# Performance work log

Measured on AMD Instinct MI355X. Metric: run time of the kernel, lower is better.

Reference implementation:

```python
import jax, jax.numpy as jnp
import numpy as np

B, N, E, H = 4, 2048, 256, 8
D = E // H
EPS = 1e-5


def _layernorm(x, g, b):
    mu = jnp.mean(x, axis=-1, keepdims=True)
    var = jnp.mean(jnp.square(x - mu), axis=-1, keepdims=True)
    return (x - mu) * jax.lax.rsqrt(var + EPS) * g + b


def setup_inputs() -> dict:
    key = jax.random.key(0)
    ks = jax.random.split(key, 8)
    s = 1.0 / np.sqrt(E)
    lin = lambda k: (jax.random.normal(k, (E, E), jnp.float32) * s)
    return {
        "x_l": jax.random.normal(ks[0], (B, N, E), jnp.float32),
        "x_r": jax.random.normal(ks[1], (B, N, E), jnp.float32),
        "Wq": lin(ks[2]), "bq": jnp.zeros((E,), jnp.float32),
        "Wk": lin(ks[3]), "bk": jnp.zeros((E,), jnp.float32),
        "Wv": lin(ks[4]), "bv": jnp.zeros((E,), jnp.float32),
        "Wp": lin(ks[5]), "bp": jnp.zeros((E,), jnp.float32),
        "ln_g": jnp.ones((E,), jnp.float32), "ln_b": jnp.zeros((E,), jnp.float32),
        "rn_g": jnp.ones((E,), jnp.float32), "rn_b": jnp.zeros((E,), jnp.float32),
    }


def reference(x_l, x_r, Wq, bq, Wk, bk, Wv, bv, Wp, bp, ln_g, ln_b, rn_g, rn_b):
    # projections -> [b, h, n, d]
    q = (x_l @ Wq + bq).reshape(B, N, H, D).transpose(0, 2, 1, 3)
    k = (x_r @ Wk + bk).reshape(B, N, H, D).transpose(0, 2, 1, 3)
    # shared value from the difference of the two streams
    v = ((x_l - x_r) @ Wv + bv).reshape(B, N, H, D).transpose(0, 2, 1, 3)

    energy = jnp.einsum('bhqd,bhkd->bhqk', q, k)  # [b,h,n,n]
    attn = jax.nn.softmax(energy / np.sqrt(D), axis=-1)  # dropout p=0 (eval)

    # attn used as-is and transposed against the SAME value tensor
    out_l = jnp.einsum('bhqk,bhkd->bhqd', attn, v)
    out_r = jnp.einsum('bhqk,bhqd->bhkd', attn, v)  # == attn^T @ v

    out_l = out_l.transpose(0, 2, 1, 3).reshape(B, N, E)
    out_r = out_r.transpose(0, 2, 1, 3).reshape(B, N, E)

    out_l = _layernorm(out_l @ Wp + bp, ln_g, ln_b) + x_l
    out_r = _layernorm(out_r @ Wp + bp, rn_g, rn_b) + x_r
    return (out_l, out_r)
```

## Files before the change

kernel.cpp:

```cpp
#include <hip/hip_runtime.h>
#include <math.h>


typedef __attribute__((ext_vector_type(8))) short short8;
typedef __attribute__((ext_vector_type(4))) float f32x4;
typedef __attribute__((ext_vector_type(16))) float f32x16;
typedef __attribute__((ext_vector_type(4))) unsigned short u16x4;

union FragU { unsigned int u[4]; short8 s8; };

__device__ __forceinline__ unsigned short bf16_rn(float f) {
    union { float f; unsigned int u; } c; c.f = f;
    return (unsigned short)((c.u + 0x7FFFu + ((c.u >> 16) & 1u)) >> 16);
}
__device__ __forceinline__ float b2f(unsigned short u) {
    union { unsigned int i; float f; } c; c.i = ((unsigned int)u) << 16;
    return c.f;
}

#if __has_builtin(__builtin_amdgcn_exp2f)
__device__ __forceinline__ float fexp2(float x) { return __builtin_amdgcn_exp2f(x); }
#else
__device__ __forceinline__ float fexp2(float x) { return exp2f(x); }
#endif

__device__ __forceinline__ f32x4 mfma16(short8 a, short8 b, f32x4 c) {
    return __builtin_amdgcn_mfma_f32_16x16x32_bf16(a, b, c, 0, 0, 0);
}
__device__ __forceinline__ f32x16 mfma32(short8 a, short8 b, f32x16 c) {
    return __builtin_amdgcn_mfma_f32_32x32x16_bf16(a, b, c, 0, 0, 0);
}

__device__ __forceinline__ void plswap(unsigned int& x, unsigned int& y) {
    asm("v_permlane32_swap_b32 %0, %1" : "+v"(x), "+v"(y));
}

__device__ __forceinline__ short8 pfrag(unsigned int w0, unsigned int w1,
                                        unsigned int w2, unsigned int w3) {
    plswap(w0, w2);
    plswap(w1, w3);
    FragU fu;
    fu.u[0] = w0; fu.u[1] = w1; fu.u[2] = w2; fu.u[3] = w3;
    return fu.s8;
}

__global__ void prep_all(const float* __restrict__ xl, const float* __restrict__ xr,
                         const float* __restrict__ Wq, const float* __restrict__ Wk,
                         const float* __restrict__ Wv, const float* __restrict__ Wp,
                         unsigned short* __restrict__ xlb, unsigned short* __restrict__ xrb,
                         unsigned short* __restrict__ xdb,
                         unsigned short* __restrict__ Wqt, unsigned short* __restrict__ Wkt,
                         unsigned short* __restrict__ Wvt, unsigned short* __restrict__ Wpt) {
    const int bid = blockIdx.x;
    if (bid < 2048) {
        const size_t i = ((size_t)bid * 256 + threadIdx.x) * 4;
        const float4 A = *(const float4*)(xl + i);
        const float4 Bv = *(const float4*)(xr + i);
        u16x4 pa = { bf16_rn(A.x), bf16_rn(A.y), bf16_rn(A.z), bf16_rn(A.w) };
        u16x4 pb = { bf16_rn(Bv.x), bf16_rn(Bv.y), bf16_rn(Bv.z), bf16_rn(Bv.w) };
        u16x4 pd = { bf16_rn(A.x - Bv.x), bf16_rn(A.y - Bv.y),
                     bf16_rn(A.z - Bv.z), bf16_rn(A.w - Bv.w) };
        *(u16x4*)(xlb + i) = pa;
        *(u16x4*)(xrb + i) = pb;
        *(u16x4*)(xdb + i) = pd;
    } else {
        const int gid = (bid - 2048) * 256 + threadIdx.x;
        const int m = gid >> 16;
        const int idx = gid & 65535;
        const int k = idx >> 8, n = idx & 255;
        const float* W = (m == 0) ? Wq : (m == 1) ? Wk : (m == 2) ? Wv : Wp;
        unsigned short* Wt = (m == 0) ? Wqt : (m == 1) ? Wkt : (m == 2) ? Wvt : Wpt;
        Wt[n * 256 + k] = bf16_rn(W[(size_t)k * 256 + n]);
    }
}

__launch_bounds__(256)
__global__ void qkv_gemm(const unsigned short* __restrict__ xlb,
                         const unsigned short* __restrict__ xrb,
                         const unsigned short* __restrict__ xdb,
                         const unsigned short* __restrict__ Wqt,
                         const unsigned short* __restrict__ Wkt,
                         const unsigned short* __restrict__ Wvt,
                         const float* __restrict__ bq, const float* __restrict__ bk,
                         const float* __restrict__ bv,
                         unsigned short* __restrict__ Qg, unsigned short* __restrict__ Kg,
                         unsigned short* __restrict__ Vtg) {
    const int z = blockIdx.z;
    const unsigned short* A  = (z == 0) ? xlb : (z == 1) ? xrb : xdb;
    const unsigned short* Wt = (z == 0) ? Wqt : (z == 1) ? Wkt : Wvt;
    const float* bias        = (z == 0) ? bq  : (z == 1) ? bk  : bv;

    __shared__ unsigned short At[2][128][40];
    __shared__ unsigned short Bt[2][64][40];

    const int tid = threadIdx.x;
    const int lane = tid & 63, wv = tid >> 6;
    const int a = lane & 15, g = lane >> 4;
    const int wr = wv >> 1, wc = wv & 1;
    const int r0 = blockIdx.x * 128;
    const int c0 = blockIdx.y * 64;

    const f32x4 fz = {0.f, 0.f, 0.f, 0.f};
    f32x4 acc[4][2];
#pragma unroll
    for (int f = 0; f < 4; ++f)
#pragma unroll
        for (int t = 0; t < 2; ++t) acc[f][t] = fz;

    const int arow = tid >> 1, aoff = (tid & 1) * 16;
    const int brow = tid >> 2, boff = (tid & 3) * 8;
    const unsigned short* asrc = A + (size_t)(r0 + arow) * 256 + aoff;
    const unsigned short* bsrc = Wt + (size_t)(c0 + brow) * 256 + boff;

#define QKV_STAGE(KS, BUF)                                                      \
    {                                                                           \
        *(short8*)&At[BUF][arow][aoff]     = *(const short8*)(asrc + (KS) * 32); \
        *(short8*)&At[BUF][arow][aoff + 8] = *(const short8*)(asrc + (KS) * 32 + 8); \
        *(short8*)&Bt[BUF][brow][boff]     = *(const short8*)(bsrc + (KS) * 32); \
    }

    QKV_STAGE(0, 0)
    __syncthreads();

#pragma unroll
    for (int ks = 0; ks < 8; ++ks) {
        const int b = ks & 1;
        if (ks < 7) QKV_STAGE(ks + 1, b ^ 1)
        short8 af[4], bfr[2];
#pragma unroll
        for (int f = 0; f < 4; ++f) af[f] = *(const short8*)&At[b][wr * 64 + f * 16 + a][g * 8];
#pragma unroll
        for (int t = 0; t < 2; ++t) bfr[t] = *(const short8*)&Bt[b][wc * 32 + t * 16 + a][g * 8];
#pragma unroll
        for (int f = 0; f < 4; ++f)
#pragma unroll
            for (int t = 0; t < 2; ++t) acc[f][t] = mfma16(af[f], bfr[t], acc[f][t]);
        __syncthreads();
    }
#undef QKV_STAGE

    const float scq = 0.17677669529663687f * 1.4426950408889634f;
#pragma unroll
    for (int t = 0; t < 2; ++t) {
        const int C = c0 + wc * 32 + t * 16 + a;
        const float bb = bias[C];
        const int h = C >> 5, d = C & 31;
#pragma unroll
        for (int f = 0; f < 4; ++f) {
            const int Rb = r0 + wr * 64 + f * 16 + g * 4;
            const int b_ = Rb >> 11, n = Rb & 2047;
            const int bhh = b_ * 8 + h;
            float v[4];
#pragma unroll
            for (int r = 0; r < 4; ++r) {
                v[r] = acc[f][t][r] + bb;
                if (z == 0) v[r] *= scq;
            }
            if (z < 2) {
                unsigned short* dst = ((z == 0) ? Qg : Kg) + (size_t)(bhh * 2048 + n) * 32 + d;
#pragma unroll
                for (int r = 0; r < 4; ++r) dst[(size_t)r * 32] = bf16_rn(v[r]);
            } else {
                u16x4 pk = { bf16_rn(v[0]), bf16_rn(v[1]), bf16_rn(v[2]), bf16_rn(v[3]) };
                *(u16x4*)(Vtg + (size_t)(bhh * 32 + d) * 2048 + n) = pk;
            }
        }
    }
}

#define P1_TILE(SB)                                                             \
    {                                                                           \
        const short8 ck0 = *(const short8*)((SB) + ro);                         \
        const short8 ck1 = *(const short8*)((SB) + 512 + ro);                   \
        const short8 cv0 = *(const short8*)((SB) + 1024 + ro);                  \
        const short8 cv1 = *(const short8*)((SB) + 1536 + ro);                  \
        f32x16 s = {};                                                          \
        s = mfma32(ck0, qf0, s);                                                \
        s = mfma32(ck1, qf1, s);                                                \
        float p[16];                                                            \
        _Pragma("unroll") for (int j = 0; j < 16; ++j) p[j] = fexp2(s[j]);      \
        l_run += (((p[0] + p[1]) + (p[2] + p[3])) + ((p[4] + p[5]) + (p[6] + p[7]))) \
               + (((p[8] + p[9]) + (p[10] + p[11])) + ((p[12] + p[13]) + (p[14] + p[15]))); \
        unsigned int w[8];                                                      \
        _Pragma("unroll") for (int mm = 0; mm < 8; ++mm)                        \
            asm("v_cvt_pk_bf16_f32 %0, %1, %2"                                  \
                : "=v"(w[mm]) : "v"(p[2 * mm]), "v"(p[2 * mm + 1]));            \
        acc = mfma32(cv0, pfrag(w[0], w[1], w[2], w[3]), acc);                  \
        acc = mfma32(cv1, pfrag(w[4], w[5], w[6], w[7]), acc);                  \
    }

__launch_bounds__(512, 4)
__global__ void attn_pass1(const unsigned short* __restrict__ Qg,
                           const unsigned short* __restrict__ Kg,
                           const unsigned short* __restrict__ Vtg,
                           unsigned short* __restrict__ AOl,
                           unsigned short* __restrict__ Vsg) {
    __shared__ unsigned short ST[2][2][2][2][2][64][8];
    __shared__ float accS[4][16][64];
    __shared__ float lsumS[4][64];

    const int f = blockIdx.x;
    const int bh = 4 * (f & 7) + (f >> 7);
    const int qblk = (f >> 3) & 15;
    const int tid = threadIdx.x;
    const int wv = tid >> 6;
    const int qi = wv & 3, z = wv >> 2;
    const int lane = tid & 63, l31 = lane & 31, hi = lane >> 5;
    const int q0 = qblk * 128 + qi * 32;

    const unsigned short* Qb = Qg + (size_t)bh * 2048 * 32;
    const unsigned short* Kb = Kg + (size_t)bh * 2048 * 32;
    const unsigned short* Vb = Vtg + (size_t)bh * 32 * 2048;

    const short8 qf0 = *(const short8*)(Qb + (size_t)(q0 + l31) * 32 + hi * 8);
    const short8 qf1 = *(const short8*)(Qb + (size_t)(q0 + l31) * 32 + 16 + hi * 8);

    const int kv = qi >> 1;
    const int srow = (qi & 1) * 16 + (lane >> 2);
    const int m = lane & 3;
    unsigned short* wp00 = &ST[z][0][0][kv][m >> 1][srow + 32 * (m & 1)][0];
    unsigned short* wp01 = &ST[z][0][1][kv][m >> 1][srow + 32 * (m & 1)][0];
    unsigned short* wp10 = &ST[z][1][0][kv][m >> 1][srow + 32 * (m & 1)][0];
    unsigned short* wp11 = &ST[z][1][1][kv][m >> 1][srow + 32 * (m & 1)][0];
    const size_t gstep = kv ? 32 : 1024;
    const unsigned short* sgb = kv
        ? Vb + (size_t)srow * 2048 + m * 8
        : Kb + (size_t)srow * 32 + m * 8;
    const int zt = z * 32;

    const unsigned short* rb00 = &ST[z][0][0][0][0][0][0];
    const unsigned short* rb01 = &ST[z][0][1][0][0][0][0];
    const unsigned short* rb10 = &ST[z][1][0][0][0][0][0];
    const unsigned short* rb11 = &ST[z][1][1][0][0][0][0];
    const int ro = (l31 + 32 * hi) * 8;

    f32x16 acc = {};
    float l_run = 0.f;

    short8 rr0 = *(const short8*)(sgb + (size_t)(zt + 0) * gstep);
    short8 rr1 = *(const short8*)(sgb + (size_t)(zt + 1) * gstep);
    *(short8*)wp00 = rr0;
    *(short8*)wp01 = rr1;
    rr0 = *(const short8*)(sgb + (size_t)(zt + 2) * gstep);
    rr1 = *(const short8*)(sgb + (size_t)(zt + 3) * gstep);
    __syncthreads();

#pragma unroll
    for (int ph = 0; ph < 16; ++ph) {
        const int pb = ph & 1;
        unsigned short* wA = pb ? wp00 : wp10;
        unsigned short* wB = pb ? wp01 : wp11;
        const unsigned short* rA = pb ? rb10 : rb00;
        const unsigned short* rB = pb ? rb11 : rb01;
        if (ph < 15) { *(short8*)wA = rr0; *(short8*)wB = rr1; }
        if (ph < 14) {
            rr0 = *(const short8*)(sgb + (size_t)(zt + 2 * ph + 4) * gstep);
            rr1 = *(const short8*)(sgb + (size_t)(zt + 2 * ph + 5) * gstep);
        }
        P1_TILE(rA)
        P1_TILE(rB)
        __syncthreads();
    }

    float lsum = l_run + __shfl_xor(l_run, 32);

    if (z == 1) {
#pragma unroll
        for (int j = 0; j < 16; ++j) accS[qi][j][lane] = acc[j];
        lsumS[qi][lane] = lsum;
    }
    __syncthreads();
    if (z == 0) {
        lsum += lsumS[qi][lane];
        const float rl = 1.0f / lsum;
#pragma unroll
        for (int j = 0; j < 16; ++j) acc[j] += accS[qi][j][lane];

        const int b_ = bh >> 3, h = bh & 7;
        const int q = q0 + l31;
        unsigned short* dst = AOl + (size_t)(b_ * 2048 + q) * 256 + h * 32;
#pragma unroll
        for (int g2 = 0; g2 < 4; ++g2) {
            u16x4 pk = { bf16_rn(acc[4 * g2 + 0] * rl), bf16_rn(acc[4 * g2 + 1] * rl),
                         bf16_rn(acc[4 * g2 + 2] * rl), bf16_rn(acc[4 * g2 + 3] * rl) };
            *(u16x4*)(dst + 8 * g2 + 4 * hi) = pk;
        }
        if (hi == 0) lsumS[qi][l31] = rl;
    }
    __syncthreads();
    if (z == 1) {
        const int cb = hi * 16;
        float il[16];
#pragma unroll
        for (int e = 0; e < 16; e += 4) {
            const float4 v4 = *(const float4*)&lsumS[qi][cb + e];
            il[e] = v4.x; il[e + 1] = v4.y; il[e + 2] = v4.z; il[e + 3] = v4.w;
        }
        const unsigned short* vsrc = Vb + (size_t)l31 * 2048 + q0 + cb;
        unsigned short* vdst = Vsg + (size_t)bh * 32 * 2048 + (size_t)l31 * 2048 + q0 + cb;
#pragma unroll
        for (int c4 = 0; c4 < 4; ++c4) {
            const u16x4 vv = *(const u16x4*)(vsrc + c4 * 4);
            u16x4 o = { bf16_rn(b2f(vv.x) * il[c4 * 4 + 0]),
                        bf16_rn(b2f(vv.y) * il[c4 * 4 + 1]),
                        bf16_rn(b2f(vv.z) * il[c4 * 4 + 2]),
                        bf16_rn(b2f(vv.w) * il[c4 * 4 + 3]) };
            *(u16x4*)(vdst + c4 * 4) = o;
        }
    }
}

#define P2_TILE(SB)                                                             \
    {                                                                           \
        const short8 cq0 = *(const short8*)((SB) + ro);                         \
        const short8 cq1 = *(const short8*)((SB) + 512 + ro);                   \
        const short8 cv0 = *(const short8*)((SB) + 1024 + ro);                  \
        const short8 cv1 = *(const short8*)((SB) + 1536 + ro);                  \
        f32x16 s = {};                                                          \
        s = mfma32(cq0, kf0, s);                                                \
        s = mfma32(cq1, kf1, s);                                                \
        float p[16];                                                            \
        _Pragma("unroll") for (int j = 0; j < 16; ++j) p[j] = fexp2(s[j]);      \
        unsigned int w[8];                                                      \
        _Pragma("unroll") for (int mm = 0; mm < 8; ++mm)                        \
            asm("v_cvt_pk_bf16_f32 %0, %1, %2"                                  \
                : "=v"(w[mm]) : "v"(p[2 * mm]), "v"(p[2 * mm + 1]));            \
        acc = mfma32(pfrag(w[0], w[1], w[2], w[3]), cv0, acc);                  \
        acc = mfma32(pfrag(w[4], w[5], w[6], w[7]), cv1, acc);                  \
    }

__launch_bounds__(512, 4)
__global__ void attn_pass2(const unsigned short* __restrict__ Qg,
                           const unsigned short* __restrict__ Kg,
                           const unsigned short* __restrict__ Vsg,
                           unsigned short* __restrict__ AOr) {
    __shared__ unsigned short ST[2][2][2][2][2][64][8];
    __shared__ float accS[4][16][64];

    const int f = blockIdx.x;
    const int bh = 4 * (f & 7) + (f >> 7);
    const int kblk = (f >> 3) & 15;
    const int tid = threadIdx.x;
    const int wv = tid >> 6;
    const int ki = wv & 3, z = wv >> 2;
    const int lane = tid & 63, l31 = lane & 31, hi = lane >> 5;
    const int k0 = kblk * 128 + ki * 32;

    const unsigned short* Qb = Qg + (size_t)bh * 2048 * 32;
    const unsigned short* Kb = Kg + (size_t)bh * 2048 * 32;
    const unsigned short* Vb = Vsg + (size_t)bh * 32 * 2048;

    const short8 kf0 = *(const short8*)(Kb + (size_t)(k0 + l31) * 32 + hi * 8);
    const short8 kf1 = *(const short8*)(Kb + (size_t)(k0 + l31) * 32 + 16 + hi * 8);

    const int kv = ki >> 1;
    const int srow = (ki & 1) * 16 + (lane >> 2);
    const int m = lane & 3;
    unsigned short* wp00 = &ST[z][0][0][kv][m >> 1][srow + 32 * (m & 1)][0];
    unsigned short* wp01 = &ST[z][0][1][kv][m >> 1][srow + 32 * (m & 1)][0];
    unsigned short* wp10 = &ST[z][1][0][kv][m >> 1][srow + 32 * (m & 1)][0];
    unsigned short* wp11 = &ST[z][1][1][kv][m >> 1][srow + 32 * (m & 1)][0];
    const size_t gstep = kv ? 32 : 1024;
    const unsigned short* sgb = kv
        ? Vb + (size_t)srow * 2048 + m * 8
        : Qb + (size_t)srow * 32 + m * 8;
    const int zt = z * 32;

    const unsigned short* rb00 = &ST[z][0][0][0][0][0][0];
    const unsigned short* rb01 = &ST[z][0][1][0][0][0][0];
    const unsigned short* rb10 = &ST[z][1][0][0][0][0][0];
    const unsigned short* rb11 = &ST[z][1][1][0][0][0][0];
    const int ro = (l31 + 32 * hi) * 8;

    f32x16 acc = {};

    short8 rr0 = *(const short8*)(sgb + (size_t)(zt + 0) * gstep);
    short8 rr1 = *(const short8*)(sgb + (size_t)(zt + 1) * gstep);
    *(short8*)wp00 = rr0;
    *(short8*)wp01 = rr1;
    rr0 = *(const short8*)(sgb + (size_t)(zt + 2) * gstep);
    rr1 = *(const short8*)(sgb + (size_t)(zt + 3) * gstep);
    __syncthreads();

#pragma unroll
    for (int ph = 0; ph < 16; ++ph) {
        const int pb = ph & 1;
        unsigned short* wA = pb ? wp00 : wp10;
        unsigned short* wB = pb ? wp01 : wp11;
        const unsigned short* rA = pb ? rb10 : rb00;
        const unsigned short* rB = pb ? rb11 : rb01;
        if (ph < 15) { *(short8*)wA = rr0; *(short8*)wB = rr1; }
        if (ph < 14) {
            rr0 = *(const short8*)(sgb + (size_t)(zt + 2 * ph + 4) * gstep);
            rr1 = *(const short8*)(sgb + (size_t)(zt + 2 * ph + 5) * gstep);
        }
        P2_TILE(rA)
        P2_TILE(rB)
        __syncthreads();
    }

    if (z == 1) {
#pragma unroll
        for (int j = 0; j < 16; ++j) accS[ki][j][lane] = acc[j];
    }
    __syncthreads();
    if (z == 0) {
#pragma unroll
        for (int j = 0; j < 16; ++j) acc[j] += accS[ki][j][lane];

        const int b_ = bh >> 3, h = bh & 7;
#pragma unroll
        for (int j = 0; j < 16; ++j) {
            const int krow = k0 + (j & 3) + 8 * (j >> 2) + 4 * hi;
            AOr[(size_t)(b_ * 2048 + krow) * 256 + h * 32 + l31] = bf16_rn(acc[j]);
        }
    }
}

__launch_bounds__(256)
__global__ void proj_ln(const unsigned short* __restrict__ AOl,
                        const unsigned short* __restrict__ AOr,
                        const unsigned short* __restrict__ Wpt,
                        const float* __restrict__ bp,
                        const float* __restrict__ ln_g, const float* __restrict__ ln_b,
                        const float* __restrict__ rn_g, const float* __restrict__ rn_b,
                        const float* __restrict__ xl, const float* __restrict__ xr,
                        float* __restrict__ out) {
    __shared__ unsigned short At[64][264];
    __shared__ unsigned short Bt[2][256][40];

    const int sel = blockIdx.y;
    const unsigned short* AO = sel ? AOr : AOl;
    const float* gamma = sel ? rn_g : ln_g;
    const float* beta  = sel ? rn_b : ln_b;
    const float* xres  = sel ? xr : xl;
    float* o = out + (size_t)sel * 8192 * 256;

    const int tid = threadIdx.x;
    const int lane = tid & 63, wv = tid >> 6;
    const int a = lane & 15, g = lane >> 4;
    const int r0 = blockIdx.x * 64;

    {
        const int row = tid >> 2, seg = (tid & 3) * 64;
        const unsigned short* src = AO + (size_t)(r0 + row) * 256 + seg;
#pragma unroll
        for (int i = 0; i < 8; ++i)
            *(short8*)&At[row][seg + i * 8] = *(const short8*)(src + i * 8);
    }
    const unsigned short* wsrc = Wpt + (size_t)tid * 256;
    {
#pragma unroll
        for (int i = 0; i < 4; ++i)
            *(short8*)&Bt[0][tid][i * 8] = *(const short8*)(wsrc + i * 8);
    }

    const f32x4 fz = {0.f, 0.f, 0.f, 0.f};
    f32x4 acc[16];
#pragma unroll
    for (int cf = 0; cf < 16; ++cf) acc[cf] = fz;

    __syncthreads();

#pragma unroll
    for (int ks = 0; ks < 8; ++ks) {
        const int b = ks & 1;
        if (ks < 7) {
#pragma unroll
            for (int i = 0; i < 4; ++i)
                *(short8*)&Bt[b ^ 1][tid][i * 8] =
                    *(const short8*)(wsrc + (ks + 1) * 32 + i * 8);
        }
        const short8 af = *(const short8*)&At[wv * 16 + a][ks * 32 + g * 8];
#pragma unroll
        for (int cf = 0; cf < 16; ++cf) {
            const short8 bfr = *(const short8*)&Bt[b][cf * 16 + a][g * 8];
            acc[cf] = mfma16(af, bfr, acc[cf]);
        }
        __syncthreads();
    }

    float bb[16], gg[16], be[16];
#pragma unroll
    for (int cf = 0; cf < 16; ++cf) {
        const int c = cf * 16 + a;
        bb[cf] = bp[c]; gg[cf] = gamma[c]; be[cf] = beta[c];
    }
#pragma unroll
    for (int r = 0; r < 4; ++r) {
        float y[16];
        float s1 = 0.f, s2 = 0.f;
#pragma unroll
        for (int cf = 0; cf < 16; ++cf) {
            y[cf] = acc[cf][r] + bb[cf];
            s1 += y[cf];
            s2 += y[cf] * y[cf];
        }
#pragma unroll
        for (int mask = 1; mask <= 8; mask <<= 1) {
            s1 += __shfl_xor(s1, mask);
            s2 += __shfl_xor(s2, mask);
        }
        const float mu = s1 * (1.0f / 256.0f);
        const float var = s2 * (1.0f / 256.0f) - mu * mu;
        const float rstd = rsqrtf(var + 1e-5f);
        const int R = r0 + wv * 16 + g * 4 + r;
#pragma unroll
        for (int cf = 0; cf < 16; ++cf) {
            const int c = cf * 16 + a;
            o[(size_t)R * 256 + c] =
                (y[cf] - mu) * rstd * gg[cf] + be[cf] + xres[(size_t)R * 256 + c];
        }
    }
}

extern "C" void kernel_launch(void* const* d_in, const int* in_sizes, int n_in,
                              void* d_out, int out_size, void* d_ws, size_t ws_size,
                              hipStream_t stream) {
    const float* x_l  = (const float*)d_in[0];
    const float* x_r  = (const float*)d_in[1];
    const float* Wq   = (const float*)d_in[2];
    const float* bq   = (const float*)d_in[3];
    const float* Wk   = (const float*)d_in[4];
    const float* bk   = (const float*)d_in[5];
    const float* Wv   = (const float*)d_in[6];
    const float* bv   = (const float*)d_in[7];
    const float* Wp   = (const float*)d_in[8];
    const float* bp   = (const float*)d_in[9];
    const float* ln_g = (const float*)d_in[10];
    const float* ln_b = (const float*)d_in[11];
    const float* rn_g = (const float*)d_in[12];
    const float* rn_b = (const float*)d_in[13];

    const size_t SZ_TOK = (size_t)8192 * 256;

    unsigned short* xl_bf = (unsigned short*)d_ws;
    unsigned short* xr_bf = xl_bf + SZ_TOK;
    unsigned short* xd_bf = xr_bf + SZ_TOK;
    unsigned short* Qg    = xd_bf + SZ_TOK;
    unsigned short* Kg    = Qg + SZ_TOK;
    unsigned short* Vtg   = Kg + SZ_TOK;
    unsigned short* Wqt   = Vtg + SZ_TOK;
    unsigned short* Wkt   = Wqt + 65536;
    unsigned short* Wvt   = Wkt + 65536;
    unsigned short* Wpt   = Wvt + 65536;
    unsigned short* AOl   = xl_bf;
    unsigned short* AOr   = xr_bf;
    unsigned short* Vs    = xd_bf;
    float* out = (float*)d_out;

    prep_all<<<3072, 256, 0, stream>>>(x_l, x_r, Wq, Wk, Wv, Wp,
                                       xl_bf, xr_bf, xd_bf, Wqt, Wkt, Wvt, Wpt);
    qkv_gemm<<<dim3(64, 4, 3), 256, 0, stream>>>(xl_bf, xr_bf, xd_bf,
                                                 Wqt, Wkt, Wvt, bq, bk, bv, Qg, Kg, Vtg);
    attn_pass1<<<512, 512, 0, stream>>>(Qg, Kg, Vtg, AOl, Vs);
    attn_pass2<<<512, 512, 0, stream>>>(Qg, Kg, Vs, AOr);
    proj_ln<<<dim3(128, 2), 256, 0, stream>>>(AOl, AOr, Wpt, bp,
                                              ln_g, ln_b, rn_g, rn_b, x_l, x_r, out);
}
```

Before: 90.37 us.

## Split proj_ln row tile across column-half waves with LDS layernorm reduction

Halves the rows per block in the output-projection+layernorm kernel (64→32) and splits the 256 output columns between pairs of waves, doubling the grid to 512 blocks. Each wave now keeps 8 accumulators instead of 16, which lowers register pressure. Layernorm partial sums are exchanged through a small shared array with an added barrier. This spreads the kernel across more CUs and may improve occupancy, at the cost of each block reloading the full Wp and one extra sync.

Measured after the change: 87.31 us, median of 3. -3.4%, faster.

```diff
diff --git a/kernel.cpp b/kernel.cpp
--- a/kernel.cpp
+++ b/kernel.cpp
@@ -426,8 +426,9 @@
                         const float* __restrict__ rn_g, const float* __restrict__ rn_b,
                         const float* __restrict__ xl, const float* __restrict__ xr,
                         float* __restrict__ out) {
-    __shared__ unsigned short At[64][264];
+    __shared__ unsigned short At[32][264];
     __shared__ unsigned short Bt[2][256][40];
+    __shared__ float lnS[2][2][2][16];
 
     const int sel = blockIdx.y;
     const unsigned short* AO = sel ? AOr : AOl;
@@ -439,26 +440,25 @@
     const int tid = threadIdx.x;
     const int lane = tid & 63, wv = tid >> 6;
     const int a = lane & 15, g = lane >> 4;
-    const int r0 = blockIdx.x * 64;
+    const int wr = wv >> 1, wc = wv & 1;
+    const int r0 = blockIdx.x * 32;
 
     {
-        const int row = tid >> 2, seg = (tid & 3) * 64;
+        const int row = tid >> 3, seg = (tid & 7) * 32;
         const unsigned short* src = AO + (size_t)(r0 + row) * 256 + seg;
 #pragma unroll
-        for (int i = 0; i < 8; ++i)
+        for (int i = 0; i < 4; ++i)
             *(short8*)&At[row][seg + i * 8] = *(const short8*)(src + i * 8);
     }
     const unsigned short* wsrc = Wpt + (size_t)tid * 256;
-    {
-#pragma unroll
-        for (int i = 0; i < 4; ++i)
-            *(short8*)&Bt[0][tid][i * 8] = *(const short8*)(wsrc + i * 8);
-    }
+#pragma unroll
+    for (int i = 0; i < 4; ++i)
+        *(short8*)&Bt[0][tid][i * 8] = *(const short8*)(wsrc + i * 8);
 
     const f32x4 fz = {0.f, 0.f, 0.f, 0.f};
-    f32x4 acc[16];
-#pragma unroll
-    for (int cf = 0; cf < 16; ++cf) acc[cf] = fz;
+    f32x4 acc[8];
+#pragma unroll
+    for (int cf = 0; cf < 8; ++cf) acc[cf] = fz;
 
     __syncthreads();
 
@@ -471,45 +471,61 @@
                 *(short8*)&Bt[b ^ 1][tid][i * 8] =
                     *(const short8*)(wsrc + (ks + 1) * 32 + i * 8);
         }
-        const short8 af = *(const short8*)&At[wv * 16 + a][ks * 32 + g * 8];
-#pragma unroll
-        for (int cf = 0; cf < 16; ++cf) {
-            const short8 bfr = *(const short8*)&Bt[b][cf * 16 + a][g * 8];
+        const short8 af = *(const short8*)&At[wr * 16 + a][ks * 32 + g * 8];
+#pragma unroll
+        for (int cf = 0; cf < 8; ++cf) {
+            const short8 bfr = *(const short8*)&Bt[b][wc * 128 + cf * 16 + a][g * 8];
             acc[cf] = mfma16(af, bfr, acc[cf]);
         }
         __syncthreads();
     }
 
-    float bb[16], gg[16], be[16];
-#pragma unroll
-    for (int cf = 0; cf < 16; ++cf) {
-        const int c = cf * 16 + a;
+    float bb[8], gg[8], be[8];
+#pragma unroll
+    for (int cf = 0; cf < 8; ++cf) {
+        const int c = wc * 128 + cf * 16 + a;
         bb[cf] = bp[c]; gg[cf] = gamma[c]; be[cf] = beta[c];
     }
+
+    float y[4][8], s1r[4], s2r[4];
 #pragma unroll
     for (int r = 0; r < 4; ++r) {
-        float y[16];
         float s1 = 0.f, s2 = 0.f;
 #pragma unroll
-        for (int cf = 0; cf < 16; ++cf) {
-            y[cf] = acc[cf][r] + bb[cf];
-            s1 += y[cf];
-            s2 += y[cf] * y[cf];
+        for (int cf = 0; cf < 8; ++cf) {
+            const float yv = acc[cf][r] + bb[cf];
+            y[r][cf] = yv;
+            s1 += yv;
+            s2 += yv * yv;
         }
 #pragma unroll
         for (int mask = 1; mask <= 8; mask <<= 1) {
             s1 += __shfl_xor(s1, mask);
             s2 += __shfl_xor(s2, mask);
         }
+        s1r[r] = s1; s2r[r] = s2;
+    }
+    if (a == 0) {
+#pragma unroll
+        for (int r = 0; r < 4; ++r) {
+            lnS[wr][wc][0][g * 4 + r] = s1r[r];
+            lnS[wr][wc][1][g * 4 + r] = s2r[r];
+        }
+    }
+    __syncthreads();
+#pragma unroll
+    for (int r = 0; r < 4; ++r) {
+        const float s1 = s1r[r] + lnS[wr][wc ^ 1][0][g * 4 + r];
+        const float s2 = s2r[r] + lnS[wr][wc ^ 1][1][g * 4 + r];
         const float mu = s1 * (1.0f / 256.0f);
         const float var = s2 * (1.0f / 256.0f) - mu * mu;
         const float rstd = rsqrtf(var + 1e-5f);
-        const int R = r0 + wv * 16 + g * 4 + r;
-#pragma unroll
-        for (int cf = 0; cf < 16; ++cf) {
-            const int c = cf * 16 + a;
+        const int R = r0 + wr * 16 + g * 4 + r;
+#pragma unroll
+        for (int cf = 0; cf < 8; ++cf) {
+            const int c = wc * 128 + cf * 16 + a;
             o[(size_t)R * 256 + c] =
-                (y[cf] - mu) * rstd * gg[cf] + be[cf] + xres[(size_t)R * 256 + c];
+                (y[r][cf] - mu) * rstd * gg[cf] + be[cf] + xres[(size_t)R * 256 + c];
         }
     }
 }
@@ -555,6 +571,6 @@
                                                  Wqt, Wkt, Wvt, bq, bk, bv, Qg, Kg, Vtg);
     attn_pass1<<<512, 512, 0, stream>>>(Qg, Kg, Vtg, AOl, Vs);
     attn_pass2<<<512, 512, 0, stream>>>(Qg, Kg, Vs, AOr);
-    proj_ln<<<dim3(128, 2), 256, 0, stream>>>(AOl, AOr, Wpt, bp,
+    proj_ln<<<dim3(256, 2), 256, 0, stream>>>(AOl, AOr, Wpt, bp,
                                               ln_g, ln_b, rn_g, rn_b, x_l, x_r, out);
 }
```
